# Performance work log

Measured on AMD Instinct MI355X. Metric: run time of the kernel, lower is better.

Reference implementation:

```python
import jax, jax.numpy as jnp
import numpy as np

N = 50000      # nodes
F_IN = 256     # nfeat
HID = 64       # nhid (per-head, layer 1)
H = 4          # heads layer 1
OUT = 64       # nhid2 (layer 2, heads=1, concat=False)
E = 800000     # edges (self-loops appended in reference)
NEG_SLOPE = 0.2  # PyG GATConv default LeakyReLU slope


def setup_inputs() -> dict:
    key = jax.random.key(0)
    ks = jax.random.split(key, 10)
    x = jax.random.normal(ks[0], (N, F_IN), dtype=jnp.float32)
    adj = jax.random.randint(ks[1], (2, E), 0, N)
    s1 = 1.0 / np.sqrt(F_IN)
    s2 = 1.0 / np.sqrt(H * HID)
    W1 = (jax.random.normal(ks[2], (F_IN, H * HID), dtype=jnp.float32) * s1)
    att_src1 = jax.random.normal(ks[3], (H, HID), dtype=jnp.float32) * 0.1
    att_dst1 = jax.random.normal(ks[4], (H, HID), dtype=jnp.float32) * 0.1
    b1 = jnp.zeros((H * HID,), dtype=jnp.float32)
    W2 = (jax.random.normal(ks[5], (H * HID, OUT), dtype=jnp.float32) * s2)
    att_src2 = jax.random.normal(ks[6], (1, OUT), dtype=jnp.float32) * 0.1
    att_dst2 = jax.random.normal(ks[7], (1, OUT), dtype=jnp.float32) * 0.1
    b2 = jnp.zeros((OUT,), dtype=jnp.float32)
    return {"x": x, "adj": adj, "W1": W1, "att_src1": att_src1,
            "att_dst1": att_dst1, "b1": b1, "W2": W2, "att_src2": att_src2,
            "att_dst2": att_dst2, "b2": b2}


def _gat_conv(x, src, dst, W, a_src, a_dst, bias, heads, out_ch, concat):
    n = x.shape[0]
    h = (x @ W).reshape(n, heads, out_ch)                    # [N, H, C]
    alpha_src = jnp.einsum('nhc,hc->nh', h, a_src)           # [N, H]
    alpha_dst = jnp.einsum('nhc,hc->nh', h, a_dst)           # [N, H]
    alpha = jax.nn.leaky_relu(alpha_src[src] + alpha_dst[dst],
                              negative_slope=NEG_SLOPE)      # [E, H]
    # segment softmax over incoming edges of each dst node
    m = jax.ops.segment_max(alpha, dst, num_segments=n)      # [N, H]
    e = jnp.exp(alpha - m[dst])
    denom = jax.ops.segment_sum(e, dst, num_segments=n)      # [N, H]
    a = e / denom[dst]                                       # [E, H]
    msg = h[src] * a[:, :, None]                             # [E, H, C]
    out = jax.ops.segment_sum(msg, dst, num_segments=n)      # [N, H, C]
    if concat:
        out = out.reshape(n, heads * out_ch)
    else:
        out = out.mean(axis=1)
    return out + bias


def reference(x, adj, W1, att_src1, att_dst1, b1, W2, att_src2, att_dst2, b2):
    loops = jnp.arange(N, dtype=adj.dtype)
    src = jnp.concatenate([adj[0], loops])
    dst = jnp.concatenate([adj[1], loops])
    h = _gat_conv(x, src, dst, W1, att_src1, att_dst1, b1, H, HID, True)
    h = jax.nn.elu(h)
    out = _gat_conv(h, src, dst, W2, att_src2, att_dst2, b2, 1, OUT, False)
    return jax.nn.log_softmax(out, axis=1)
```

## Files before the change

kernel.cpp:

```cpp
#include <hip/hip_runtime.h>
#include <cstdint>
#include <cstddef>

#define NN    50000
#define EE    800000
#define SLOPE 0.2f
#define MT64  782
#define CAP   64

#define NBIN  391
#define PBLK  512
#define EPB   1563
#define BCAP  24
#define OCAP  8192

typedef unsigned short ushortT;
typedef __attribute__((ext_vector_type(8))) short short8;
typedef __attribute__((ext_vector_type(4))) float floatx4;

__device__ __forceinline__ float lrelu(float x){ return x > 0.f ? x : SLOPE * x; }
__device__ __forceinline__ float eluf(float x){ return x > 0.f ? x : __expf(x) - 1.f; }
__device__ __forceinline__ ushortT f2b(float f){ unsigned u = __float_as_uint(f); u += 0x7fff + ((u >> 16) & 1); return (ushortT)(u >> 16); }
__device__ __forceinline__ float   b2f(ushortT b){ return __uint_as_float(((unsigned)b) << 16); }

__global__ __launch_bounds__(256) void binCast_k(const int* __restrict__ srcA,
                                                 const int* __restrict__ dstA,
                                                 unsigned* __restrict__ binned,
                                                 ushortT* __restrict__ cnt2,
                                                 unsigned* __restrict__ ovf,
                                                 int* __restrict__ ovfcnt,
                                                 const float* __restrict__ W1,
                                                 const float* __restrict__ W2,
                                                 ushortT* __restrict__ W1T,
                                                 ushortT* __restrict__ W2T)
{
    __shared__ int      hist[NBIN];
    __shared__ unsigned lrec[NBIN][BCAP];
    if (blockIdx.x >= PBLK) {
        int k = blockIdx.x - PBLK, t = threadIdx.x;
        W1T[t * 256 + k] = f2b(W1[k * 256 + t]);
        if (t < 64) W2T[t * 256 + k] = f2b(W2[k * 64 + t]);
        return;
    }
    const int blk = blockIdx.x;
    const int tid = threadIdx.x;
    for (int i = tid; i < NBIN; i += 256) hist[i] = 0;
    __syncthreads();

    const int e0 = blk * EPB;
    const int e1 = min(e0 + EPB, EE);
    for (int e = e0 + tid; e < e1; e += 256) {
        int s = srcA[e], d = dstA[e];
        int bin = d >> 7;
        unsigned rec = ((unsigned)s << 7) | (unsigned)(d & 127);
        int r = atomicAdd(&hist[bin], 1);
        if (r < BCAP) lrec[bin][r] = rec;
        else {
            int o = atomicAdd(ovfcnt, 1);
            if (o < OCAP) ovf[o] = ((unsigned)s << 16) | (unsigned)d;
        }
    }
    __syncthreads();

    for (int b = tid; b < NBIN; b += 256)
        cnt2[(size_t)blk * NBIN + b] = (ushortT)min(hist[b], BCAP);
    for (int sIdx = tid; sIdx < NBIN * BCAP; sIdx += 256) {
        int b = sIdx / BCAP;
        int i = sIdx - b * BCAP;
        if (i < min(hist[b], BCAP))
            binned[((size_t)b * PBLK + blk) * BCAP + i] = lrec[b][i];
    }
}

__global__ __launch_bounds__(256) void gemm1_k(const float* __restrict__ x,
                                               const ushortT* __restrict__ W1T,
                                               const float* __restrict__ attS,
                                               const float* __restrict__ attD,
                                               ushortT* __restrict__ h1b,
                                               float* __restrict__ asrc,
                                               float* __restrict__ adst)
{
    const int tid  = threadIdx.x;
    const int w    = tid >> 6;
    const int lane = tid & 63;
    const int m16  = lane & 15;
    const int quad = lane >> 4;
    const int wr   = w >> 1;
    const int wc   = w & 1;
    const int rowbase = blockIdx.x * 64 + wr * 32;
    const int colbase = wc * 128;

    const long r0 = min(rowbase + m16,      NN - 1);
    const long r1 = min(rowbase + 16 + m16, NN - 1);
    const float* a0p = x + r0 * 256 + quad * 8;
    const float* a1p = x + r1 * 256 + quad * 8;
    const ushortT* bp0 = W1T + (size_t)(colbase + m16) * 256 + quad * 8;

    floatx4 acc[2][8];
    #pragma unroll
    for (int i = 0; i < 2; ++i)
        #pragma unroll
        for (int j = 0; j < 8; ++j) acc[i][j] = (floatx4){0.f, 0.f, 0.f, 0.f};

    #pragma unroll
    for (int it = 0; it < 8; ++it) {
        const int k0 = it * 32;
        float4 fa00 = *(const float4*)(a0p + k0);
        float4 fa01 = *(const float4*)(a0p + k0 + 4);
        float4 fa10 = *(const float4*)(a1p + k0);
        float4 fa11 = *(const float4*)(a1p + k0 + 4);
        uint4 fb[8];
        #pragma unroll
        for (int j = 0; j < 8; ++j)
            fb[j] = *(const uint4*)(bp0 + (size_t)j * 16 * 256 + k0);

        ushortT a16[16];
        a16[0]=f2b(fa00.x); a16[1]=f2b(fa00.y); a16[2]=f2b(fa00.z); a16[3]=f2b(fa00.w);
        a16[4]=f2b(fa01.x); a16[5]=f2b(fa01.y); a16[6]=f2b(fa01.z); a16[7]=f2b(fa01.w);
        a16[8]=f2b(fa10.x); a16[9]=f2b(fa10.y); a16[10]=f2b(fa10.z); a16[11]=f2b(fa10.w);
        a16[12]=f2b(fa11.x); a16[13]=f2b(fa11.y); a16[14]=f2b(fa11.z); a16[15]=f2b(fa11.w);
        short8 af0 = *(short8*)(a16);
        short8 af1 = *(short8*)(a16 + 8);

        #pragma unroll
        for (int j = 0; j < 8; ++j) {
            short8 bf = *(short8*)(&fb[j]);
            acc[0][j] = __builtin_amdgcn_mfma_f32_16x16x32_bf16(af0, bf, acc[0][j], 0, 0, 0);
            acc[1][j] = __builtin_amdgcn_mfma_f32_16x16x32_bf16(af1, bf, acc[1][j], 0, 0, 0);
        }
    }

    float attSv[8], attDv[8];
    #pragma unroll
    for (int j = 0; j < 8; ++j) {
        attSv[j] = attS[colbase + j * 16 + m16];
        attDv[j] = attD[colbase + j * 16 + m16];
    }

    #pragma unroll
    for (int i = 0; i < 2; ++i) {
        #pragma unroll
        for (int r = 0; r < 4; ++r) {
            int row = rowbase + i * 16 + quad * 4 + r;
            bool ok = row < NN;
            if (ok) {
                #pragma unroll
                for (int j = 0; j < 8; ++j)
                    h1b[(size_t)row * 256 + colbase + j * 16 + m16] = f2b(acc[i][j][r]);
            }
            float d0 = 0.f, d1 = 0.f, e0 = 0.f, e1 = 0.f;
            #pragma unroll
            for (int jj = 0; jj < 4; ++jj) {
                d0 += acc[i][jj][r]     * attSv[jj];
                e0 += acc[i][jj][r]     * attDv[jj];
                d1 += acc[i][jj + 4][r] * attSv[jj + 4];
                e1 += acc[i][jj + 4][r] * attDv[jj + 4];
            }
            #pragma unroll
            for (int off = 1; off < 16; off <<= 1) {
                d0 += __shfl_xor(d0, off); e0 += __shfl_xor(e0, off);
                d1 += __shfl_xor(d1, off); e1 += __shfl_xor(e1, off);
            }
            if (ok && m16 == 0) {
                int hb = row * 4 + wc * 2;
                asrc[hb] = d0; asrc[hb + 1] = d1;
                adst[hb] = e0; adst[hb + 1] = e1;
            }
        }
    }
}

__global__ __launch_bounds__(256) void bucket_k(const unsigned* __restrict__ binned,
                                                const ushortT* __restrict__ cnt2,
                                                const unsigned* __restrict__ ovf,
                                                const int* __restrict__ ovfcnt,
                                                ushortT* __restrict__ esorted,
                                                int* __restrict__ cnt)
{
    __shared__ ushortT c2[PBLK];
    __shared__ int     lcnt[128];
    __shared__ ushortT lbuck[128][CAP];
    const int b = blockIdx.x;
    const int tid = threadIdx.x;

    for (int i = tid; i < 128; i += 256) lcnt[i] = 0;
    for (int i = tid; i < PBLK; i += 256) c2[i] = cnt2[(size_t)i * NBIN + b];
    __syncthreads();

    for (int s0 = tid; s0 < PBLK * BCAP; s0 += 1024) {
        unsigned recs[4]; int ok[4];
        #pragma unroll
        for (int q = 0; q < 4; ++q) {
            int s = s0 + q * 256;
            int blk = s / BCAP;
            int i = s - blk * BCAP;
            ok[q] = (i < (int)c2[blk]);
            recs[q] = ok[q] ? binned[((size_t)b * PBLK + blk) * BCAP + i] : 0u;
        }
        #pragma unroll
        for (int q = 0; q < 4; ++q) {
            if (ok[q]) {
                int dl = recs[q] & 127;
                int r = atomicAdd(&lcnt[dl], 1);
                if (r < CAP) lbuck[dl][r] = (ushortT)(recs[q] >> 7);
            }
        }
    }

    int nov = *ovfcnt;
    nov = nov > OCAP ? OCAP : nov;
    for (int i = tid; i < nov; i += 256) {
        unsigned rec = ovf[i];
        int d = rec & 0xFFFF;
        if ((d >> 7) == b) {
            int r = atomicAdd(&lcnt[d & 127], 1);
            if (r < CAP) lbuck[d & 127][r] = (ushortT)(rec >> 16);
        }
    }
    __syncthreads();

    const int nbase = b << 7;
    if (tid < 128) {
        int n = nbase + tid;
        if (n < NN) cnt[n] = lcnt[tid];
    }
    unsigned* ed = (unsigned*)(esorted + (size_t)nbase * CAP);
    const unsigned* ls = (const unsigned*)(&lbuck[0][0]);
    for (int i = tid; i < 128 * (CAP / 2); i += 256) {
        if (nbase + (i >> 5) < NN) ed[i] = ls[i];
    }
}

__global__ __launch_bounds__(256) void gemm2_k(const ushortT* __restrict__ a2b,
                                               const ushortT* __restrict__ W2T,
                                               const float* __restrict__ attS,
                                               const float* __restrict__ attD,
                                               ushortT* __restrict__ t2b,
                                               float* __restrict__ asrc,
                                               float* __restrict__ adst)
{
    const int tid  = threadIdx.x;
    const int w    = tid >> 6;
    const int lane = tid & 63;
    const int m16  = lane & 15;
    const int quad = lane >> 4;
    const int rowbase = blockIdx.x * 64 + w * 16;

    const long r0 = min(rowbase + m16, NN - 1);
    const ushortT* ap  = a2b + r0 * 256 + quad * 8;
    const ushortT* bp0 = W2T + (size_t)m16 * 256 + quad * 8;

    floatx4 acc[4];
    #pragma unroll
    for (int j = 0; j < 4; ++j) acc[j] = (floatx4){0.f, 0.f, 0.f, 0.f};

    #pragma unroll
    for (int it = 0; it < 8; ++it) {
        const int k0 = it * 32;
        uint4 fa = *(const uint4*)(ap + k0);
        uint4 fb[4];
        #pragma unroll
        for (int j = 0; j < 4; ++j)
            fb[j] = *(const uint4*)(bp0 + (size_t)j * 16 * 256 + k0);
        short8 af = *(short8*)(&fa);
        #pragma unroll
        for (int j = 0; j < 4; ++j) {
            short8 bf = *(short8*)(&fb[j]);
            acc[j] = __builtin_amdgcn_mfma_f32_16x16x32_bf16(af, bf, acc[j], 0, 0, 0);
        }
    }

    float attSv[4], attDv[4];
    #pragma unroll
    for (int j = 0; j < 4; ++j) {
        attSv[j] = attS[j * 16 + m16];
        attDv[j] = attD[j * 16 + m16];
    }

    #pragma unroll
    for (int r = 0; r < 4; ++r) {
        int row = rowbase + quad * 4 + r;
        bool ok = row < NN;
        if (ok) {
            #pragma unroll
            for (int j = 0; j < 4; ++j)
                t2b[(size_t)row * 64 + j * 16 + m16] = f2b(acc[j][r]);
        }
        float ds = 0.f, dd = 0.f;
        #pragma unroll
        for (int j = 0; j < 4; ++j) {
            ds += acc[j][r] * attSv[j];
            dd += acc[j][r] * attDv[j];
        }
        #pragma unroll
        for (int off = 1; off < 16; off <<= 1) {
            ds += __shfl_xor(ds, off);
            dd += __shfl_xor(dd, off);
        }
        if (ok && m16 == 0) {
            asrc[row] = ds;
            adst[row] = dd;
        }
    }
}

__global__ __launch_bounds__(256) void agg1_k(const ushortT* __restrict__ esorted,
                                              const int* __restrict__ cnt,
                                              const ushortT* __restrict__ h1b,
                                              const float* __restrict__ asrc,
                                              const float* __restrict__ adst,
                                              const float* __restrict__ b1,
                                              ushortT* __restrict__ a2b)
{
    __shared__ float pbuf[4][64][4];
    __shared__ int   sbuf[4][64];
    int w = threadIdx.x >> 6;
    int lane = threadIdx.x & 63;
    int n = blockIdx.x * 4 + w;
    if (n >= NN) return;
    int start = n * CAP;
    int deg = min(cnt[n], CAP);
    float4 adv = *(const float4*)(adst + (size_t)n * 4);
    float4 asf = *(const float4*)(asrc + (size_t)n * 4);
    int h = lane >> 4;
    int c4 = lane * 4;

    float4 pself;
    pself.x = __expf(lrelu(asf.x + adv.x));
    pself.y = __expf(lrelu(asf.y + adv.y));
    pself.z = __expf(lrelu(asf.z + adv.z));
    pself.w = __expf(lrelu(asf.w + adv.w));
    float psh = (h < 2) ? (h == 0 ? pself.x : pself.y) : (h == 2 ? pself.z : pself.w);

    ushort4 hsv = *(const ushort4*)(h1b + (size_t)n * 256 + c4);
    float4 ac0 = make_float4(b2f(hsv.x) * psh, b2f(hsv.y) * psh, b2f(hsv.z) * psh, b2f(hsv.w) * psh);
    float4 ac1 = make_float4(0.f,0.f,0.f,0.f);
    float4 ac2 = make_float4(0.f,0.f,0.f,0.f);
    float4 ac3 = make_float4(0.f,0.f,0.f,0.f);
    float4 ssv = make_float4(0.f, 0.f, 0.f, 0.f);

    for (int base = 0; base < deg; base += 64) {
        int cl = min(64, deg - base);
        int i = base + lane;
        if (i < deg) {
            int s = esorted[start + i];
            float4 a = *(const float4*)(asrc + (size_t)s * 4);
            float4 pv;
            pv.x = __expf(lrelu(a.x + adv.x));
            pv.y = __expf(lrelu(a.y + adv.y));
            pv.z = __expf(lrelu(a.z + adv.z));
            pv.w = __expf(lrelu(a.w + adv.w));
            ssv.x += pv.x; ssv.y += pv.y; ssv.z += pv.z; ssv.w += pv.w;
            *(float4*)(&pbuf[w][lane][0]) = pv;
            sbuf[w][lane] = s;
        }
        __builtin_amdgcn_wave_barrier();
        int j = 0;
        for (; j + 7 < cl; j += 8) {
            float4 hv[8]; float pp[8];
            #pragma unroll
            for (int q = 0; q < 8; ++q) {
                int sq = sbuf[w][j + q];
                pp[q] = pbuf[w][j + q][h];
                ushort4 hq = *(const ushort4*)(h1b + (size_t)sq * 256 + c4);
                hv[q] = make_float4(b2f(hq.x), b2f(hq.y), b2f(hq.z), b2f(hq.w));
            }
            #pragma unroll
            for (int q = 0; q < 8; ++q) {
                float4* ac = (q & 3) == 0 ? &ac0 : (q & 3) == 1 ? &ac1 : (q & 3) == 2 ? &ac2 : &ac3;
                ac->x += hv[q].x * pp[q]; ac->y += hv[q].y * pp[q];
                ac->z += hv[q].z * pp[q]; ac->w += hv[q].w * pp[q];
            }
        }
        for (; j < cl; ++j) {
            int s0 = sbuf[w][j];
            float p0 = pbuf[w][j][h];
            ushort4 h0 = *(const ushort4*)(h1b + (size_t)s0 * 256 + c4);
            ac0.x += b2f(h0.x) * p0; ac0.y += b2f(h0.y) * p0; ac0.z += b2f(h0.z) * p0; ac0.w += b2f(h0.w) * p0;
        }
        __builtin_amdgcn_wave_barrier();
    }

    #pragma unroll
    for (int off = 1; off < 64; off <<= 1) {
        ssv.x += __shfl_xor(ssv.x, off); ssv.y += __shfl_xor(ssv.y, off);
        ssv.z += __shfl_xor(ssv.z, off); ssv.w += __shfl_xor(ssv.w, off);
    }
    float ssh = (h < 2) ? (h == 0 ? ssv.x : ssv.y) : (h == 2 ? ssv.z : ssv.w);
    float rdh = 1.f / (ssh + psh);

    float4 bv = *(const float4*)(b1 + c4);
    ushort4 o;
    o.x = f2b(eluf((ac0.x + ac1.x + ac2.x + ac3.x) * rdh + bv.x));
    o.y = f2b(eluf((ac0.y + ac1.y + ac2.y + ac3.y) * rdh + bv.y));
    o.z = f2b(eluf((ac0.z + ac1.z + ac2.z + ac3.z) * rdh + bv.z));
    o.w = f2b(eluf((ac0.w + ac1.w + ac2.w + ac3.w) * rdh + bv.w));
    *(ushort4*)(a2b + (size_t)n * 256 + c4) = o;
}

__global__ __launch_bounds__(256) void agg2_k(const ushortT* __restrict__ esorted,
                                              const int* __restrict__ cnt,
                                              const ushortT* __restrict__ t2b,
                                              const float* __restrict__ asrc,
                                              const float* __restrict__ adst,
                                              const float* __restrict__ b2,
                                              float* __restrict__ out)
{
    __shared__ float pbuf[4][64];
    __shared__ int   sbuf[4][64];
    int w = threadIdx.x >> 6;
    int lane = threadIdx.x & 63;
    int n = blockIdx.x * 4 + w;
    if (n >= NN) return;
    int start = n * CAP;
    int deg = min(cnt[n], CAP);
    float adv = adst[n];

    float pself = __expf(lrelu(asrc[n] + adv));
    float a0 = b2f(t2b[(size_t)n * 64 + lane]) * pself;
    float a1 = 0.f, a2 = 0.f, a3 = 0.f;
    float ss = 0.f;

    for (int base = 0; base < deg; base += 64) {
        int cl = min(64, deg - base);
        int i = base + lane;
        if (i < deg) {
            int s = esorted[start + i];
            float p = __expf(lrelu(asrc[s] + adv));
            ss += p;
            pbuf[w][lane] = p;
            sbuf[w][lane] = s;
        }
        __builtin_amdgcn_wave_barrier();
        int j = 0;
        for (; j + 7 < cl; j += 8) {
            float tv[8]; float pp[8];
            #pragma unroll
            for (int q = 0; q < 8; ++q) {
                int sq = sbuf[w][j + q];
                pp[q] = pbuf[w][j + q];
                tv[q] = b2f(t2b[(size_t)sq * 64 + lane]);
            }
            #pragma unroll
            for (int q = 0; q < 8; ++q) {
                float* ac = (q & 3) == 0 ? &a0 : (q & 3) == 1 ? &a1 : (q & 3) == 2 ? &a2 : &a3;
                *ac += tv[q] * pp[q];
            }
        }
        for (; j < cl; ++j) {
            a0 += b2f(t2b[(size_t)sbuf[w][j] * 64 + lane]) * pbuf[w][j];
        }
        __builtin_amdgcn_wave_barrier();
    }

    #pragma unroll
    for (int off = 1; off < 64; off <<= 1) ss += __shfl_xor(ss, off);
    float v = (a0 + a1 + a2 + a3) / (ss + pself) + b2[lane];

    float m2 = v;
    #pragma unroll
    for (int off = 32; off; off >>= 1) m2 = fmaxf(m2, __shfl_xor(m2, off));
    float ex = __expf(v - m2);
    float sm = ex;
    #pragma unroll
    for (int off = 32; off; off >>= 1) sm += __shfl_xor(sm, off);
    out[(size_t)n * 64 + lane] = v - m2 - __logf(sm);
}

extern "C" void kernel_launch(void* const* d_in, const int* in_sizes, int n_in,
                              void* d_out, int out_size, void* d_ws, size_t ws_size,
                              hipStream_t stream)
{
    const float* x   = (const float*)d_in[0];
    const int*   adj = (const int*)  d_in[1];
    const float* W1  = (const float*)d_in[2];
    const float* as1 = (const float*)d_in[3];
    const float* ad1 = (const float*)d_in[4];
    const float* b1  = (const float*)d_in[5];
    const float* W2  = (const float*)d_in[6];
    const float* as2 = (const float*)d_in[7];
    const float* ad2 = (const float*)d_in[8];
    const float* b2  = (const float*)d_in[9];
    float* out = (float*)d_out;

    const size_t szH1b = (size_t)NN * 256 * 2;
    const size_t szT2b = (size_t)NN * 64 * 2;
    const size_t szA4  = (size_t)NN * 4 * 4;
    const size_t szA1  = (size_t)NN * 4;
    const size_t szE   = (size_t)NN * CAP * 2;
    const size_t szBin = (size_t)NBIN * PBLK * BCAP * 4;
    const size_t szC2  = (size_t)PBLK * NBIN * 2;

    char* p = (char*)d_ws;
    ushortT* h1b  = (ushortT*)p; p += szH1b;
    ushortT* a2b  = (ushortT*)p; p += szH1b;
    ushortT* t2b  = (ushortT*)p; p += szT2b;
    ushortT* W1T  = (ushortT*)p; p += 256 * 256 * 2;
    ushortT* W2T  = (ushortT*)p; p += 64 * 256 * 2;
    float* asrc1  = (float*)p; p += szA4;
    float* adst1  = (float*)p; p += szA4;
    float* asrc2  = (float*)p; p += szA1;
    float* adst2  = (float*)p; p += szA1;
    ushortT* esorted = (ushortT*)p; p += szE;
    int* cnt      = (int*)p; p += szA1;
    unsigned* binned = (unsigned*)p; p += szBin;
    ushortT* cnt2 = (ushortT*)p; p += szC2;
    unsigned* ovf = (unsigned*)p; p += (size_t)OCAP * 4;
    int* ovfcnt   = (int*)p; p += 64;

    const int nwb = (NN + 3) / 4;

    hipMemsetAsync(ovfcnt, 0, sizeof(int), stream);

    binCast_k<<<PBLK + 256, 256, 0, stream>>>(adj, adj + EE, binned, cnt2, ovf, ovfcnt,
                                              W1, W2, W1T, W2T);

    bucket_k<<<NBIN, 256, 0, stream>>>(binned, cnt2, ovf, ovfcnt, esorted, cnt);

    gemm1_k<<<MT64, 256, 0, stream>>>(x, W1T, as1, ad1, h1b, asrc1, adst1);

    agg1_k<<<nwb, 256, 0, stream>>>(esorted, cnt, h1b, asrc1, adst1, b1, a2b);
    gemm2_k<<<MT64, 256, 0, stream>>>(a2b, W2T, as2, ad2, t2b, asrc2, adst2);
    agg2_k<<<nwb, 256, 0, stream>>>(esorted, cnt, t2b, asrc2, adst2, b2, out);
}
```

Baseline: 290.7 us.

## Double-buffer neighbor gathers in aggregation kernels and tighten bin capacity

Both aggregation kernels now preload up to 64 neighbor indices and weights in one pass, padding unused slots with zero weight. The row gathers are then software-pipelined over fixed batches of 8, with two register buffers so the next batch's loads are in flight while the current batch is accumulated. This removes the per-8 tail loop. The change also lowers the per-bin capacity in the binning kernel, which spills more edges to the overflow path, and adds an occupancy hint of 3 blocks to gemm1_k. Double buffering raises register pressure in the aggregation kernels.

```diff
diff --git a/kernel.cpp b/kernel.cpp
--- a/kernel.cpp
+++ b/kernel.cpp
@@ -11,7 +11,7 @@
 #define NBIN  391
 #define PBLK  512
 #define EPB   1563
-#define BCAP  24
+#define BCAP  16
 #define OCAP  8192
 
 typedef unsigned short ushortT;
@@ -72,13 +72,13 @@
     }
 }
 
-__global__ __launch_bounds__(256) void gemm1_k(const float* __restrict__ x,
-                                               const ushortT* __restrict__ W1T,
-                                               const float* __restrict__ attS,
-                                               const float* __restrict__ attD,
-                                               ushortT* __restrict__ h1b,
-                                               float* __restrict__ asrc,
-                                               float* __restrict__ adst)
+__global__ __launch_bounds__(256, 3) void gemm1_k(const float* __restrict__ x,
+                                                  const ushortT* __restrict__ W1T,
+                                                  const float* __restrict__ attS,
+                                                  const float* __restrict__ attD,
+                                                  ushortT* __restrict__ h1b,
+                                                  float* __restrict__ asrc,
+                                                  float* __restrict__ adst)
 {
     const int tid  = threadIdx.x;
     const int w    = tid >> 6;
@@ -319,7 +319,7 @@
     int n = blockIdx.x * 4 + w;
     if (n >= NN) return;
     int start = n * CAP;
-    int deg = min(cnt[n], CAP);
+    int deg = min(max(cnt[n], 0), CAP);
     float4 adv = *(const float4*)(adst + (size_t)n * 4);
     float4 asf = *(const float4*)(asrc + (size_t)n * 4);
     int h = lane >> 4;
@@ -339,47 +339,52 @@
     float4 ac3 = make_float4(0.f,0.f,0.f,0.f);
     float4 ssv = make_float4(0.f, 0.f, 0.f, 0.f);
 
-    for (int base = 0; base < deg; base += 64) {
-        int cl = min(64, deg - base);
-        int i = base + lane;
-        if (i < deg) {
-            int s = esorted[start + i];
-            float4 a = *(const float4*)(asrc + (size_t)s * 4);
-            float4 pv;
-            pv.x = __expf(lrelu(a.x + adv.x));
-            pv.y = __expf(lrelu(a.y + adv.y));
-            pv.z = __expf(lrelu(a.z + adv.z));
-            pv.w = __expf(lrelu(a.w + adv.w));
-            ssv.x += pv.x; ssv.y += pv.y; ssv.z += pv.z; ssv.w += pv.w;
-            *(float4*)(&pbuf[w][lane][0]) = pv;
-            sbuf[w][lane] = s;
-        }
-        __builtin_amdgcn_wave_barrier();
-        int j = 0;
-        for (; j + 7 < cl; j += 8) {
-            float4 hv[8]; float pp[8];
-            #pragma unroll
-            for (int q = 0; q < 8; ++q) {
-                int sq = sbuf[w][j + q];
-                pp[q] = pbuf[w][j + q][h];
-                ushort4 hq = *(const ushort4*)(h1b + (size_t)sq * 256 + c4);
-                hv[q] = make_float4(b2f(hq.x), b2f(hq.y), b2f(hq.z), b2f(hq.w));
-            }
-            #pragma unroll
-            for (int q = 0; q < 8; ++q) {
-                float4* ac = (q & 3) == 0 ? &ac0 : (q & 3) == 1 ? &ac1 : (q & 3) == 2 ? &ac2 : &ac3;
-                ac->x += hv[q].x * pp[q]; ac->y += hv[q].y * pp[q];
-                ac->z += hv[q].z * pp[q]; ac->w += hv[q].w * pp[q];
-            }
-        }
-        for (; j < cl; ++j) {
-            int s0 = sbuf[w][j];
-            float p0 = pbuf[w][j][h];
-            ushort4 h0 = *(const ushort4*)(h1b + (size_t)s0 * 256 + c4);
-            ac0.x += b2f(h0.x) * p0; ac0.y += b2f(h0.y) * p0; ac0.z += b2f(h0.z) * p0; ac0.w += b2f(h0.w) * p0;
-        }
-        __builtin_amdgcn_wave_barrier();
-    }
+    if (lane < deg) {
+        int s = esorted[start + lane];
+        float4 a = *(const float4*)(asrc + (size_t)s * 4);
+        float4 pv;
+        pv.x = __expf(lrelu(a.x + adv.x));
+        pv.y = __expf(lrelu(a.y + adv.y));
+        pv.z = __expf(lrelu(a.z + adv.z));
+        pv.w = __expf(lrelu(a.w + adv.w));
+        ssv = pv;
+        *(float4*)(&pbuf[w][lane][0]) = pv;
+        sbuf[w][lane] = s;
+    } else {
+        *(float4*)(&pbuf[w][lane][0]) = make_float4(0.f, 0.f, 0.f, 0.f);
+        sbuf[w][lane] = 0;
+    }
+    __builtin_amdgcn_wave_barrier();
+
+    int nb = (deg + 7) >> 3;
+    ushort4 bufA[8], bufB[8];
+
+#define LOADR(BUF, J0) { _Pragma("unroll") for (int q = 0; q < 8; ++q) { \
+        int sq = sbuf[w][(J0) + q]; \
+        BUF[q] = *(const ushort4*)(h1b + (size_t)sq * 256 + c4); } }
+#define CONSR(BUF, J0) { _Pragma("unroll") for (int q = 0; q < 8; ++q) { \
+        float p = pbuf[w][(J0) + q][h]; \
+        float4* ac = (q & 3) == 0 ? &ac0 : (q & 3) == 1 ? &ac1 : (q & 3) == 2 ? &ac2 : &ac3; \
+        ac->x += b2f(BUF[q].x) * p; ac->y += b2f(BUF[q].y) * p; \
+        ac->z += b2f(BUF[q].z) * p; ac->w += b2f(BUF[q].w) * p; } }
+
+    if (nb > 0) {
+        LOADR(bufA, 0)
+        #pragma unroll
+        for (int b = 0; b < 8; ++b) {
+            const int j0 = b << 3;
+            if (b & 1) {
+                if (b + 1 < nb) LOADR(bufA, j0 + 8)
+                CONSR(bufB, j0)
+            } else {
+                if (b + 1 < nb) LOADR(bufB, j0 + 8)
+                CONSR(bufA, j0)
+            }
+            if (b + 1 >= nb) break;
+        }
+    }
+#undef LOADR
+#undef CONSR
 
     #pragma unroll
     for (int off = 1; off < 64; off <<= 1) {
@@ -413,7 +418,7 @@
     int n = blockIdx.x * 4 + w;
     if (n >= NN) return;
     int start = n * CAP;
-    int deg = min(cnt[n], CAP);
+    int deg = min(max(cnt[n], 0), CAP);
     float adv = adst[n];
 
     float pself = __expf(lrelu(asrc[n] + adv));
@@ -421,37 +426,46 @@
     float a1 = 0.f, a2 = 0.f, a3 = 0.f;
     float ss = 0.f;
 
-    for (int base = 0; base < deg; base += 64) {
-        int cl = min(64, deg - base);
-        int i = base + lane;
-        if (i < deg) {
-            int s = esorted[start + i];
-            float p = __expf(lrelu(asrc[s] + adv));
-            ss += p;
-            pbuf[w][lane] = p;
-            sbuf[w][lane] = s;
-        }
-        __builtin_amdgcn_wave_barrier();
-        int j = 0;
-        for (; j + 7 < cl; j += 8) {
-            float tv[8]; float pp[8];
-            #pragma unroll
-            for (int q = 0; q < 8; ++q) {
-                int sq = sbuf[w][j + q];
-                pp[q] = pbuf[w][j + q];
-                tv[q] = b2f(t2b[(size_t)sq * 64 + lane]);
-            }
-            #pragma unroll
-            for (int q = 0; q < 8; ++q) {
-                float* ac = (q & 3) == 0 ? &a0 : (q & 3) == 1 ? &a1 : (q & 3) == 2 ? &a2 : &a3;
-                *ac += tv[q] * pp[q];
-            }
-        }
-        for (; j < cl; ++j) {
-            a0 += b2f(t2b[(size_t)sbuf[w][j] * 64 + lane]) * pbuf[w][j];
-        }
-        __builtin_amdgcn_wave_barrier();
-    }
+    if (lane < deg) {
+        int s = esorted[start + lane];
+        float p = __expf(lrelu(asrc[s] + adv));
+        ss = p;
+        pbuf[w][lane] = p;
+        sbuf[w][lane] = s;
+    } else {
+        pbuf[w][lane] = 0.f;
+        sbuf[w][lane] = 0;
+    }
+    __builtin_amdgcn_wave_barrier();
+
+    int nb = (deg + 7) >> 3;
+    ushortT bufA[8], bufB[8];
+
+#define LOADR2(BUF, J0) { _Pragma("unroll") for (int q = 0; q < 8; ++q) { \
+        int sq = sbuf[w][(J0) + q]; \
+        BUF[q] = t2b[(size_t)sq * 64 + lane]; } }
+#define CONSR2(BUF, J0) { _Pragma("unroll") for (int q = 0; q < 8; ++q) { \
+        float p = pbuf[w][(J0) + q]; \
+        float* ac = (q & 3) == 0 ? &a0 : (q & 3) == 1 ? &a1 : (q & 3) == 2 ? &a2 : &a3; \
+        *ac += b2f(BUF[q]) * p; } }
+
+    if (nb > 0) {
+        LOADR2(bufA, 0)
+        #pragma unroll
+        for (int b = 0; b < 8; ++b) {
+            const int j0 = b << 3;
+            if (b & 1) {
+                if (b + 1 < nb) LOADR2(bufA, j0 + 8)
+                CONSR2(bufB, j0)
+            } else {
+                if (b + 1 < nb) LOADR2(bufB, j0 + 8)
+                CONSR2(bufA, j0)
+            }
+            if (b + 1 >= nb) break;
+        }
+    }
+#undef LOADR2
+#undef CONSR2
 
     #pragma unroll
     for (int off = 1; off < 64; off <<= 1) ss += __shfl_xor(ss, off);
```

Result: faster. 279.6 us (-3.8%).
